# Kernel tuning notes

Measured on AMD Instinct MI355X. Metric: run time of the kernel, lower is better.

Reference implementation:

```python
import jax, jax.numpy as jnp
import numpy as np


def setup_inputs() -> dict:
    key = jax.random.key(0)
    k1, k2 = jax.random.split(key)
    images = jax.random.normal(k1, (32, 512, 32, 32), dtype=jnp.float32)
    atts = jax.random.normal(k2, (32, 512, 512), dtype=jnp.float32)
    return {"images": images, "atts": atts}


def reference(images, atts):
    # Original: softmax over last dim of atts, then broadcast-multiply
    # [N,C,C,H,W] and sum over dim=2 -> equivalent to per-sample matmul:
    # out[n,c,h,w] = sum_d softmax(atts)[n,c,d] * images[n,d,h,w]
    w = jax.nn.softmax(atts, axis=-1)          # [N,C,C]
    return jnp.einsum('ncd,ndhw->nchw', w, images)
```

## Files before the change

kernel.cpp:

```cpp
#include <hip/hip_runtime.h>
#include <stdint.h>

typedef __attribute__((ext_vector_type(4))) float  f32x4;
typedef __attribute__((ext_vector_type(8))) __bf16 bf16x8;

#define NB   32
#define CC   512
#define DD   512
#define HW   1024
#define NKS  16

#define WAITL()  asm volatile("s_waitcnt lgkmcnt(0)" ::: "memory")
#define BARR()   do { asm volatile("" ::: "memory"); __builtin_amdgcn_s_barrier(); \
                      asm volatile("" ::: "memory"); } while (0)

__global__ __launch_bounds__(512, 2) void fused_kernel(
        const float* __restrict__ images, const float* __restrict__ atts,
        float* __restrict__ out) {
    __shared__ unsigned short lA[128][512];
    __shared__ unsigned short lB[8][4][64][8];

    const int b  = blockIdx.x;
    const int g  = b & 7;
    const int q  = b >> 3;
    const int n  = (q & 3) * 8 + g;
    const int t  = q >> 2;
    const int rt = t & 3;
    const int ct = t >> 2;

    const int tid  = threadIdx.x;
    const int lane = tid & 63;
    const int w    = tid >> 6;
    const int r15  = lane & 15;
    const int kgl  = lane >> 4;

    const float* gAt = atts + (size_t)n * CC * DD + (size_t)(rt * 128) * DD;
    const float* gB  = images + (size_t)n * DD * HW + ct * 512 + w * 64;
    float*       gO  = out + (size_t)n * CC * HW + (size_t)(rt * 128) * HW
                           + ct * 512 + w * 64;

    {
        const int grp = tid >> 4;
        const int l16 = tid & 15;
        for (int s = 0; s < 4; ++s) {
            const int row = grp * 4 + s;
            const float* ap = gAt + (size_t)row * DD + l16 * 32;
            f32x4 v[8];
            #pragma unroll
            for (int j = 0; j < 8; ++j) v[j] = *(const f32x4*)(ap + j * 4);
            float m = v[0][0];
            #pragma unroll
            for (int j = 0; j < 8; ++j)
                #pragma unroll
                for (int c = 0; c < 4; ++c) m = fmaxf(m, v[j][c]);
            #pragma unroll
            for (int k = 1; k < 16; k <<= 1) m = fmaxf(m, __shfl_xor(m, k, 16));
            float sum = 0.f;
            #pragma unroll
            for (int j = 0; j < 8; ++j)
                #pragma unroll
                for (int c = 0; c < 4; ++c) {
                    v[j][c] = __expf(v[j][c] - m);
                    sum += v[j][c];
                }
            #pragma unroll
            for (int k = 1; k < 16; k <<= 1) sum += __shfl_xor(sum, k, 16);
            const float inv = 1.0f / sum;
            #pragma unroll
            for (int p = 0; p < 4; ++p) {
                bf16x8 wv;
                #pragma unroll
                for (int e = 0; e < 8; ++e)
                    wv[e] = (__bf16)(v[p * 2 + (e >> 2)][e & 3] * inv);
                const int slot = (l16 * 4 + p) ^ (row & 7);
                *(bf16x8*)&lA[row][slot * 8] = wv;
            }
        }
    }
    WAITL();
    BARR();

    f32x4  acc[8][4] = {};
    f32x4  breg[8];

    auto load_b = [&](int kt) {
        const float* p = gB + (size_t)(kt * 32 + kgl * 8) * HW + r15 * 4;
        #pragma unroll
        for (int j = 0; j < 8; ++j)
            breg[j] = *(const f32x4*)(p + (size_t)j * HW);
    };
    auto write_b = [&]() {
        #pragma unroll
        for (int cc = 0; cc < 4; ++cc) {
            bf16x8 wv;
            #pragma unroll
            for (int j = 0; j < 8; ++j) wv[j] = (__bf16)breg[j][cc];
            const int c  = r15 * 4 + cc;
            const int cs = c ^ ((c >> 3) & 3);
            *(bf16x8*)&lB[w][kgl][cs][0] = wv;
        }
    };
    auto compute = [&](int kt) {
        bf16x8 af[8], bv[4];
        #pragma unroll
        for (int m = 0; m < 8; ++m) {
            const int row  = m * 16 + r15;
            const int slot = ((kt << 2) + kgl) ^ (r15 & 7);
            af[m] = *(const bf16x8*)&lA[row][slot * 8];
        }
        #pragma unroll
        for (int nf = 0; nf < 4; ++nf) {
            const int c  = nf * 16 + r15;
            const int cs = c ^ ((c >> 3) & 3);
            bv[nf] = *(const bf16x8*)&lB[w][kgl][cs][0];
        }
        #pragma unroll
        for (int m = 0; m < 8; ++m)
            #pragma unroll
            for (int nf = 0; nf < 4; ++nf)
                acc[m][nf] = __builtin_amdgcn_mfma_f32_16x16x32_bf16(
                    af[m], bv[nf], acc[m][nf], 0, 0, 0);
    };

    load_b(0);
    write_b();
    for (int kt = 0; kt < NKS; ++kt) {
        if (kt + 1 < NKS) load_b(kt + 1);
        compute(kt);
        if (kt + 1 < NKS) write_b();
    }

    #pragma unroll
    for (int m = 0; m < 8; ++m)
        #pragma unroll
        for (int nf = 0; nf < 4; ++nf)
            #pragma unroll
            for (int r = 0; r < 4; ++r) {
                const int row = m * 16 + kgl * 4 + r;
                const int col = nf * 16 + r15;
                gO[(size_t)row * HW + col] = acc[m][nf][r];
            }
}

extern "C" void kernel_launch(void* const* d_in, const int* in_sizes, int n_in,
                              void* d_out, int out_size, void* d_ws, size_t ws_size,
                              hipStream_t stream) {
    const float* images = (const float*)d_in[0];
    const float* atts   = (const float*)d_in[1];
    float*       out    = (float*)d_out;

    fused_kernel<<<dim3(NB * 8), dim3(512), 0, stream>>>(images, atts, out);
}
```

Before: 40.08 us.

## Split softmax stats into separate kernel and stream A tiles through double-buffered LDS

```diff
diff --git a/kernel.cpp b/kernel.cpp
--- a/kernel.cpp
+++ b/kernel.cpp
@@ -14,19 +14,47 @@
 #define BARR()   do { asm volatile("" ::: "memory"); __builtin_amdgcn_s_barrier(); \
                       asm volatile("" ::: "memory"); } while (0)
 
-__global__ __launch_bounds__(512, 2) void fused_kernel(
+__global__ __launch_bounds__(256) void stats_kernel(
+        const float* __restrict__ atts, float2* __restrict__ stats) {
+    const int row = blockIdx.x * 16 + (threadIdx.x >> 4);
+    const int l16 = threadIdx.x & 15;
+    const float* a = atts + (size_t)row * DD + l16 * 32;
+
+    f32x4 v[8];
+    #pragma unroll
+    for (int j = 0; j < 8; ++j) v[j] = *(const f32x4*)(a + j * 4);
+
+    float m = v[0][0];
+    #pragma unroll
+    for (int j = 0; j < 8; ++j)
+        #pragma unroll
+        for (int c = 0; c < 4; ++c) m = fmaxf(m, v[j][c]);
+    #pragma unroll
+    for (int s = 1; s < 16; s <<= 1) m = fmaxf(m, __shfl_xor(m, s, 16));
+
+    float sum = 0.f;
+    #pragma unroll
+    for (int j = 0; j < 8; ++j)
+        #pragma unroll
+        for (int c = 0; c < 4; ++c) sum += __expf(v[j][c] - m);
+    #pragma unroll
+    for (int s = 1; s < 16; s <<= 1) sum += __shfl_xor(sum, s, 16);
+
+    if (l16 == 0) stats[row] = make_float2(m, 1.0f / sum);
+}
+
+__global__ __launch_bounds__(256, 2) void fused_kernel(
         const float* __restrict__ images, const float* __restrict__ atts,
-        float* __restrict__ out) {
-    __shared__ unsigned short lA[128][512];
-    __shared__ unsigned short lB[8][4][64][8];
+        const float2* __restrict__ stats, float* __restrict__ out) {
+    __shared__ unsigned short lA[2][128][36];
+    __shared__ unsigned short lB[4][4][64][8];
 
     const int b  = blockIdx.x;
     const int g  = b & 7;
     const int q  = b >> 3;
-    const int n  = (q & 3) * 8 + g;
-    const int t  = q >> 2;
-    const int rt = t & 3;
-    const int ct = t >> 2;
+    const int n  = (q >> 4) * 8 + g;
+    const int rt = (q & 15) >> 2;
+    const int ct = q & 3;
 
     const int tid  = threadIdx.x;
     const int lane = tid & 63;
@@ -34,62 +62,43 @@
     const int r15  = lane & 15;
     const int kgl  = lane >> 4;
 
-    const float* gAt = atts + (size_t)n * CC * DD + (size_t)(rt * 128) * DD;
-    const float* gB  = images + (size_t)n * DD * HW + ct * 512 + w * 64;
-    float*       gO  = out + (size_t)n * CC * HW + (size_t)(rt * 128) * HW
-                           + ct * 512 + w * 64;
+    const float*  gAt = atts + (size_t)n * CC * DD + (size_t)(rt * 128) * DD;
+    const float*  gB  = images + (size_t)n * DD * HW + ct * 256 + w * 64;
+    float*        gO  = out + (size_t)n * CC * HW + (size_t)(rt * 128) * HW
+                            + ct * 256 + w * 64;
 
-    {
-        const int grp = tid >> 4;
-        const int l16 = tid & 15;
-        for (int s = 0; s < 4; ++s) {
-            const int row = grp * 4 + s;
-            const float* ap = gAt + (size_t)row * DD + l16 * 32;
-            f32x4 v[8];
+    const int arow  = tid >> 1;
+    const int ahalf = tid & 1;
+    const float2 st = stats[(size_t)n * CC + rt * 128 + arow];
+
+    f32x4 a4[4];
+    f32x4 breg[8];
+    f32x4 acc[8][4] = {};
+
+    auto loadAt = [&](int kt) {
+        const float* p = gAt + (size_t)arow * DD + kt * 32 + ahalf * 16;
+        #pragma unroll
+        for (int j = 0; j < 4; ++j) a4[j] = *(const f32x4*)(p + j * 4);
+    };
+    auto stageA = [&](int buf) {
+        #pragma unroll
+        for (int u = 0; u < 2; ++u) {
+            bf16x8 wv;
             #pragma unroll
-            for (int j = 0; j < 8; ++j) v[j] = *(const f32x4*)(ap + j * 4);
-            float m = v[0][0];
-            #pragma unroll
-            for (int j = 0; j < 8; ++j)
-                #pragma unroll
-                for (int c = 0; c < 4; ++c) m = fmaxf(m, v[j][c]);
-            #pragma unroll
-            for (int k = 1; k < 16; k <<= 1) m = fmaxf(m, __shfl_xor(m, k, 16));
-            float sum = 0.f;
-            #pragma unroll
-            for (int j = 0; j < 8; ++j)
-                #pragma unroll
-                for (int c = 0; c < 4; ++c) {
-                    v[j][c] = __expf(v[j][c] - m);
-                    sum += v[j][c];
-                }
-            #pragma unroll
-            for (int k = 1; k < 16; k <<= 1) sum += __shfl_xor(sum, k, 16);
-            const float inv = 1.0f / sum;
-            #pragma unroll
-            for (int p = 0; p < 4; ++p) {
-                bf16x8 wv;
-                #pragma unroll
-                for (int e = 0; e < 8; ++e)
-                    wv[e] = (__bf16)(v[p * 2 + (e >> 2)][e & 3] * inv);
-                const int slot = (l16 * 4 + p) ^ (row & 7);
-                *(bf16x8*)&lA[row][slot * 8] = wv;
+            for (int e = 0; e < 8; ++e) {
+                const float x = a4[u * 2 + (e >> 2)][e & 3];
+                wv[e] = (__bf16)(__expf(x - st.x) * st.y);
             }
+            *(bf16x8*)&lA[buf][arow][(ahalf * 2 + u) * 8] = wv;
         }
-    }
-    WAITL();
-    BARR();
-
-    f32x4  acc[8][4] = {};
-    f32x4  breg[8];
-
-    auto load_b = [&](int kt) {
+    };
+    auto loadB = [&](int kt) {
         const float* p = gB + (size_t)(kt * 32 + kgl * 8) * HW + r15 * 4;
         #pragma unroll
         for (int j = 0; j < 8; ++j)
             breg[j] = *(const f32x4*)(p + (size_t)j * HW);
     };
-    auto write_b = [&]() {
+    auto writeB = [&]() {
         #pragma unroll
         for (int cc = 0; cc < 4; ++cc) {
             bf16x8 wv;
@@ -100,14 +109,11 @@
             *(bf16x8*)&lB[w][kgl][cs][0] = wv;
         }
     };
-    auto compute = [&](int kt) {
+    auto compute = [&](int buf) {
         bf16x8 af[8], bv[4];
         #pragma unroll
-        for (int m = 0; m < 8; ++m) {
-            const int row  = m * 16 + r15;
-            const int slot = ((kt << 2) + kgl) ^ (r15 & 7);
-            af[m] = *(const bf16x8*)&lA[row][slot * 8];
-        }
+        for (int m = 0; m < 8; ++m)
+            af[m] = *(const bf16x8*)&lA[buf][m * 16 + r15][kgl * 8];
         #pragma unroll
         for (int nf = 0; nf < 4; ++nf) {
             const int c  = nf * 16 + r15;
@@ -122,12 +128,24 @@
                     af[m], bv[nf], acc[m][nf], 0, 0, 0);
     };
 
-    load_b(0);
-    write_b();
+    loadAt(0);
+    loadB(0);
+    stageA(0);
+    writeB();
+    loadAt(1);
+    loadB(1);
+    WAITL();
+    BARR();
+
+    #pragma unroll
     for (int kt = 0; kt < NKS; ++kt) {
-        if (kt + 1 < NKS) load_b(kt + 1);
-        compute(kt);
-        if (kt + 1 < NKS) write_b();
+        const int cur = kt & 1, nxt = cur ^ 1;
+        if (kt + 1 < NKS) stageA(nxt);
+        if (kt + 2 < NKS) loadAt(kt + 2);
+        compute(cur);
+        if (kt + 1 < NKS) writeB();
+        if (kt + 2 < NKS) loadB(kt + 2);
+        if (kt + 1 < NKS) { WAITL(); BARR(); }
     }
 
     #pragma unroll
@@ -148,6 +166,8 @@
     const float* images = (const float*)d_in[0];
     const float* atts   = (const float*)d_in[1];
     float*       out    = (float*)d_out;
+    float2*      stats  = (float2*)d_ws;
 
-    fused_kernel<<<dim3(NB * 8), dim3(512), 0, stream>>>(images, atts, out);
+    stats_kernel<<<dim3(NB * CC / 16), dim3(256), 0, stream>>>(atts, stats);
+    fused_kernel<<<dim3(512), dim3(256), 0, stream>>>(images, atts, stats, out);
 }
```

Measured after the change: 46.60 us. 16.3% more time.

## Stream softmax weights per k-tile with row stats and smaller tiles

Applied to the files above, without the earlier changes.

```diff
diff --git a/kernel.cpp b/kernel.cpp
--- a/kernel.cpp
+++ b/kernel.cpp
@@ -14,19 +14,18 @@
 #define BARR()   do { asm volatile("" ::: "memory"); __builtin_amdgcn_s_barrier(); \
                       asm volatile("" ::: "memory"); } while (0)
 
-__global__ __launch_bounds__(512, 2) void fused_kernel(
+__global__ __launch_bounds__(512, 4) void fused_kernel(
         const float* __restrict__ images, const float* __restrict__ atts,
         float* __restrict__ out) {
-    __shared__ unsigned short lA[128][512];
-    __shared__ unsigned short lB[8][4][64][8];
+    __shared__ unsigned short lA[2][128][40];
+    __shared__ float2 lStats[128];
 
     const int b  = blockIdx.x;
     const int g  = b & 7;
     const int q  = b >> 3;
-    const int n  = (q & 3) * 8 + g;
-    const int t  = q >> 2;
-    const int rt = t & 3;
-    const int ct = t >> 2;
+    const int n  = (q >> 4) * 8 + g;
+    const int rt = (q >> 2) & 3;
+    const int ct = q & 3;
 
     const int tid  = threadIdx.x;
     const int lane = tid & 63;
@@ -35,13 +34,14 @@
     const int kgl  = lane >> 4;
 
     const float* gAt = atts + (size_t)n * CC * DD + (size_t)(rt * 128) * DD;
-    const float* gB  = images + (size_t)n * DD * HW + ct * 512 + w * 64;
+    const float* gB  = images + (size_t)n * DD * HW + ct * 256 + w * 32;
     float*       gO  = out + (size_t)n * CC * HW + (size_t)(rt * 128) * HW
-                           + ct * 512 + w * 64;
+                           + ct * 256 + w * 32;
 
     {
         const int grp = tid >> 4;
         const int l16 = tid & 15;
+        #pragma unroll
         for (int s = 0; s < 4; ++s) {
             const int row = grp * 4 + s;
             const float* ap = gAt + (size_t)row * DD + l16 * 32;
@@ -59,81 +59,87 @@
             #pragma unroll
             for (int j = 0; j < 8; ++j)
                 #pragma unroll
-                for (int c = 0; c < 4; ++c) {
-                    v[j][c] = __expf(v[j][c] - m);
-                    sum += v[j][c];
-                }
+                for (int c = 0; c < 4; ++c) sum += __expf(v[j][c] - m);
             #pragma unroll
             for (int k = 1; k < 16; k <<= 1) sum += __shfl_xor(sum, k, 16);
-            const float inv = 1.0f / sum;
-            #pragma unroll
-            for (int p = 0; p < 4; ++p) {
-                bf16x8 wv;
-                #pragma unroll
-                for (int e = 0; e < 8; ++e)
-                    wv[e] = (__bf16)(v[p * 2 + (e >> 2)][e & 3] * inv);
-                const int slot = (l16 * 4 + p) ^ (row & 7);
-                *(bf16x8*)&lA[row][slot * 8] = wv;
-            }
+            if (l16 == 0) lStats[row] = make_float2(m, 1.0f / sum);
         }
     }
     WAITL();
     BARR();
 
-    f32x4  acc[8][4] = {};
-    f32x4  breg[8];
+    const int arow = tid >> 2;
+    const int aq   = tid & 3;
+    const float2 st = lStats[arow];
 
-    auto load_b = [&](int kt) {
-        const float* p = gB + (size_t)(kt * 32 + kgl * 8) * HW + r15 * 4;
+    f32x4 acc[8][2] = {};
+    f32x4 areg[2];
+    float bA[16], bB[16];
+
+    auto loadAt = [&](int kt) {
+        const float* p = gAt + (size_t)arow * DD + kt * 32 + aq * 8;
+        areg[0] = *(const f32x4*)p;
+        areg[1] = *(const f32x4*)(p + 4);
+    };
+    auto stageA = [&](int buf) {
+        bf16x8 wv;
         #pragma unroll
-        for (int j = 0; j < 8; ++j)
-            breg[j] = *(const f32x4*)(p + (size_t)j * HW);
+        for (int e = 0; e < 8; ++e) {
+            const float x = areg[e >> 2][e & 3];
+            wv[e] = (__bf16)(__expf(x - st.x) * st.y);
+        }
+        *(bf16x8*)&lA[buf][arow][aq * 8] = wv;
     };
-    auto write_b = [&]() {
+    auto loadB = [&](int kt, float (&d)[16]) {
+        const float* p = gB + (size_t)(kt * 32 + kgl * 8) * HW + r15;
         #pragma unroll
-        for (int cc = 0; cc < 4; ++cc) {
-            bf16x8 wv;
+        for (int nf = 0; nf < 2; ++nf)
             #pragma unroll
-            for (int j = 0; j < 8; ++j) wv[j] = (__bf16)breg[j][cc];
-            const int c  = r15 * 4 + cc;
-            const int cs = c ^ ((c >> 3) & 3);
-            *(bf16x8*)&lB[w][kgl][cs][0] = wv;
+            for (int e = 0; e < 8; ++e)
+                d[nf * 8 + e] = p[(size_t)e * HW + nf * 16];
+    };
+    auto compute = [&](int buf, const float (&d)[16]) {
+        bf16x8 bv[2];
+        #pragma unroll
+        for (int nf = 0; nf < 2; ++nf)
+            #pragma unroll
+            for (int e = 0; e < 8; ++e)
+                bv[nf][e] = (__bf16)d[nf * 8 + e];
+        #pragma unroll
+        for (int m = 0; m < 8; ++m) {
+            const bf16x8 af = *(const bf16x8*)&lA[buf][m * 16 + r15][kgl * 8];
+            acc[m][0] = __builtin_amdgcn_mfma_f32_16x16x32_bf16(af, bv[0], acc[m][0], 0, 0, 0);
+            acc[m][1] = __builtin_amdgcn_mfma_f32_16x16x32_bf16(af, bv[1], acc[m][1], 0, 0, 0);
         }
     };
-    auto compute = [&](int kt) {
-        bf16x8 af[8], bv[4];
-        #pragma unroll
-        for (int m = 0; m < 8; ++m) {
-            const int row  = m * 16 + r15;
-            const int slot = ((kt << 2) + kgl) ^ (r15 & 7);
-            af[m] = *(const bf16x8*)&lA[row][slot * 8];
+
+    loadB(0, bA);
+    loadAt(0);
+    stageA(0);
+    loadB(1, bB);
+    loadAt(1);
+    WAITL();
+    BARR();
+
+    #pragma unroll
+    for (int kt = 0; kt < NKS; ++kt) {
+        const int cur = kt & 1, nxt = cur ^ 1;
+        if (kt + 1 < NKS) stageA(nxt);
+        if (kt + 2 < NKS) loadAt(kt + 2);
+        if (kt & 1) {
+            compute(cur, bB);
+            if (kt + 2 < NKS) loadB(kt + 2, bB);
+        } else {
+            compute(cur, bA);
+            if (kt + 2 < NKS) loadB(kt + 2, bA);
         }
-        #pragma unroll
-        for (int nf = 0; nf < 4; ++nf) {
-            const int c  = nf * 16 + r15;
-            const int cs = c ^ ((c >> 3) & 3);
-            bv[nf] = *(const bf16x8*)&lB[w][kgl][cs][0];
-        }
-        #pragma unroll
-        for (int m = 0; m < 8; ++m)
-            #pragma unroll
-            for (int nf = 0; nf < 4; ++nf)
-                acc[m][nf] = __builtin_amdgcn_mfma_f32_16x16x32_bf16(
-                    af[m], bv[nf], acc[m][nf], 0, 0, 0);
-    };
-
-    load_b(0);
-    write_b();
-    for (int kt = 0; kt < NKS; ++kt) {
-        if (kt + 1 < NKS) load_b(kt + 1);
-        compute(kt);
-        if (kt + 1 < NKS) write_b();
+        if (kt + 1 < NKS) { WAITL(); BARR(); }
     }
 
     #pragma unroll
     for (int m = 0; m < 8; ++m)
         #pragma unroll
-        for (int nf = 0; nf < 4; ++nf)
+        for (int nf = 0; nf < 2; ++nf)
             #pragma unroll
             for (int r = 0; r < 4; ++r) {
                 const int row = m * 16 + kgl * 4 + r;
@@ -149,5 +155,5 @@
     const float* atts   = (const float*)d_in[1];
     float*       out    = (float*)d_out;
 
-    fused_kernel<<<dim3(NB * 8), dim3(512), 0, stream>>>(images, atts, out);
+    fused_kernel<<<dim3(512), dim3(512), 0, stream>>>(images, atts, out);
 }
```

Measured after the change: 53.61 us. +33.8%, slower.

## Double-buffer image register prefetch, coalesce softmax loads, reswizzle B LDS

Applied to the files above, without the earlier changes.

```diff
diff --git a/kernel.cpp b/kernel.cpp
--- a/kernel.cpp
+++ b/kernel.cpp
@@ -44,10 +44,13 @@
         const int l16 = tid & 15;
         for (int s = 0; s < 4; ++s) {
             const int row = grp * 4 + s;
-            const float* ap = gAt + (size_t)row * DD + l16 * 32;
+            const float* ap = gAt + (size_t)row * DD;
             f32x4 v[8];
             #pragma unroll
-            for (int j = 0; j < 8; ++j) v[j] = *(const f32x4*)(ap + j * 4);
+            for (int p = 0; p < 4; ++p) {
+                v[2*p]   = *(const f32x4*)(ap + (p * 16 + l16) * 8);
+                v[2*p+1] = *(const f32x4*)(ap + (p * 16 + l16) * 8 + 4);
+            }
             float m = v[0][0];
             #pragma unroll
             for (int j = 0; j < 8; ++j)
@@ -71,8 +74,8 @@
                 bf16x8 wv;
                 #pragma unroll
                 for (int e = 0; e < 8; ++e)
-                    wv[e] = (__bf16)(v[p * 2 + (e >> 2)][e & 3] * inv);
-                const int slot = (l16 * 4 + p) ^ (row & 7);
+                    wv[e] = (__bf16)(v[2*p + (e >> 2)][e & 3] * inv);
+                const int slot = (p * 16 + l16) ^ (row & 7);
                 *(bf16x8*)&lA[row][slot * 8] = wv;
             }
         }
@@ -80,39 +83,37 @@
     WAITL();
     BARR();
 
-    f32x4  acc[8][4] = {};
-    f32x4  breg[8];
+    f32x4 acc[8][4] = {};
+    f32x4 bA[8], bB[8];
 
-    auto load_b = [&](int kt) {
+    auto loadB = [&](int kt, f32x4 (&d)[8]) {
         const float* p = gB + (size_t)(kt * 32 + kgl * 8) * HW + r15 * 4;
         #pragma unroll
         for (int j = 0; j < 8; ++j)
-            breg[j] = *(const f32x4*)(p + (size_t)j * HW);
+            d[j] = *(const f32x4*)(p + (size_t)j * HW);
     };
-    auto write_b = [&]() {
+    auto writeB = [&](const f32x4 (&d)[8]) {
         #pragma unroll
         for (int cc = 0; cc < 4; ++cc) {
             bf16x8 wv;
             #pragma unroll
-            for (int j = 0; j < 8; ++j) wv[j] = (__bf16)breg[j][cc];
-            const int c  = r15 * 4 + cc;
-            const int cs = c ^ ((c >> 3) & 3);
-            *(bf16x8*)&lB[w][kgl][cs][0] = wv;
+            for (int j = 0; j < 8; ++j) wv[j] = (__bf16)d[j][cc];
+            const int slot = cc * 16 + (r15 ^ (cc << 2));
+            *(bf16x8*)&lB[w][kgl][slot][0] = wv;
         }
     };
     auto compute = [&](int kt) {
         bf16x8 af[8], bv[4];
         #pragma unroll
         for (int m = 0; m < 8; ++m) {
-            const int row  = m * 16 + r15;
             const int slot = ((kt << 2) + kgl) ^ (r15 & 7);
-            af[m] = *(const bf16x8*)&lA[row][slot * 8];
+            af[m] = *(const bf16x8*)&lA[m * 16 + r15][slot * 8];
         }
         #pragma unroll
         for (int nf = 0; nf < 4; ++nf) {
-            const int c  = nf * 16 + r15;
-            const int cs = c ^ ((c >> 3) & 3);
-            bv[nf] = *(const bf16x8*)&lB[w][kgl][cs][0];
+            const int c    = nf * 16 + r15;
+            const int slot = (c & 3) * 16 + (((c >> 2) ^ ((c & 3) << 2)) & 15);
+            bv[nf] = *(const bf16x8*)&lB[w][kgl][slot][0];
         }
         #pragma unroll
         for (int m = 0; m < 8; ++m)
@@ -122,12 +123,21 @@
                     af[m], bv[nf], acc[m][nf], 0, 0, 0);
     };
 
-    load_b(0);
-    write_b();
+    loadB(0, bA);
+    loadB(1, bB);
+    writeB(bA);
+    #pragma unroll
     for (int kt = 0; kt < NKS; ++kt) {
-        if (kt + 1 < NKS) load_b(kt + 1);
         compute(kt);
-        if (kt + 1 < NKS) write_b();
+        if (kt + 1 < NKS) {
+            if (kt & 1) {
+                writeB(bA);
+                if (kt + 2 < NKS) loadB(kt + 2, bB);
+            } else {
+                writeB(bB);
+                if (kt + 2 < NKS) loadB(kt + 2, bA);
+            }
+        }
     }
 
     #pragma unroll
```

After: 35.92 us, median of 2. 10.4% less time.
